# Performance work log

Hardware: AMD Instinct MI355X
Metric: run time of the kernel (lower is better)

Reference implementation:

```python
import jax, jax.numpy as jnp
import numpy as np

K = 3
TOPK = 10
HORIZON = 12


def gru_cell(x, h, w_ih, w_hh, b_ih, b_hh):
    # torch GRU gate order: r, z, n ; n = tanh(W_in x + b_in + r*(W_hn h + b_hn))
    gx = x @ w_ih.T + b_ih
    gh = h @ w_hh.T + b_hh
    H = h.shape[-1]
    r = jax.nn.sigmoid(gx[:, :H] + gh[:, :H])
    z = jax.nn.sigmoid(gx[:, H:2 * H] + gh[:, H:2 * H])
    n = jnp.tanh(gx[:, 2 * H:] + r * gh[:, 2 * H:])
    return (1.0 - z) * n + z * h


def setup_inputs() -> dict:
    key = jax.random.key(0)
    ks = jax.random.split(key, 16)
    B, T, N, F = 128, 12, 207, 14
    H = 128
    f = lambda i, shp, s=0.1: jax.random.normal(ks[i], shp, dtype=jnp.float32) * s
    return {
        'x': jax.random.normal(ks[0], (B, T, N, F), dtype=jnp.float32),
        'A_physical': jax.random.uniform(ks[1], (N, N), dtype=jnp.float32),
        'fc_start_w': f(2, (16, 1), 0.5),
        'fc_start_b': jnp.zeros((16,), jnp.float32),
        'alpha': jnp.float32(0.5),
        'context_w': f(3, (32, 13)),
        'context_b': jnp.zeros((32,), jnp.float32),
        'tcn_w': f(4, (64, 1, 1, 3), 0.3),
        'tcn_b': jnp.zeros((64,), jnp.float32),
        'theta': f(5, (K, 32, 32), 0.15),
        'attn_w': f(6, (1, 65)),
        'attn_b': jnp.zeros((1,), jnp.float32),
        'enc_w_ih': f(7, (3 * H, 65)),
        'enc_w_hh': f(8, (3 * H, H)),
        'enc_b_ih': jnp.zeros((3 * H,), jnp.float32),
        'enc_b_hh': jnp.zeros((3 * H,), jnp.float32),
        'dec_w_ih': f(9, (3 * H, 33)),
        'dec_w_hh': f(10, (3 * H, H)),
        'dec_b_ih': jnp.zeros((3 * H,), jnp.float32),
        'dec_b_hh': jnp.zeros((3 * H,), jnp.float32),
        'out_w': f(11, (1, H)),
        'out_b': jnp.zeros((1,), jnp.float32),
    }


def reference(x, A_physical, fc_start_w, fc_start_b, alpha, context_w, context_b,
              tcn_w, tcn_b, theta, attn_w, attn_b,
              enc_w_ih, enc_w_hh, enc_b_ih, enc_b_hh,
              dec_w_ih, dec_w_hh, dec_b_ih, dec_b_hh, out_w, out_b):
    B, T, N, _ = x.shape
    H = enc_w_hh.shape[1]
    traffic = x[..., 0:1]          # [B,T,N,1]
    context = x[..., 1:]           # [B,T,N,13]

    # ---- dynamic graph: topk + scatter + softmax, blended with physical ----
    state = traffic[:, -1]                                   # [B,N,1]
    emb = jnp.tanh(state @ fc_start_w.T + fc_start_b)        # [B,N,16]
    A_dyn = jax.nn.relu(jnp.einsum('bnd,bmd->bnm', emb, emb))
    vals, idx = jax.lax.top_k(A_dyn, TOPK)
    sparse = jnp.zeros_like(A_dyn).at[
        jnp.arange(B)[:, None, None], jnp.arange(N)[None, :, None], idx].set(vals)
    A_dyn = jax.nn.softmax(sparse, axis=2)
    a = jax.nn.sigmoid(alpha)
    A = a * A_physical[None] + (1.0 - a) * A_dyn             # [B,N,N]

    # ---- gated temporal conv (causal, GLU) ----
    xt = jnp.transpose(traffic, (0, 3, 2, 1))                # [B,1,N,T]
    conv = jax.lax.conv_general_dilated(
        xt, tcn_w, (1, 1), [(0, 0), (2, 0)],
        dimension_numbers=('NCHW', 'OIHW', 'NCHW')) + tcn_b[None, :, None, None]
    P, Q = jnp.split(conv, 2, axis=1)
    t_feat = jnp.transpose(P * jax.nn.sigmoid(Q), (0, 3, 2, 1))  # [B,T,N,32]

    # ---- Chebyshev K-hop graph conv ----
    I = jnp.eye(N, dtype=x.dtype)
    lam = jnp.clip(jnp.max(jnp.sum(A, -1), -1), 1.0)[:, None, None]
    L = 2.0 * A / lam - I[None]
    Tk = [jnp.broadcast_to(I[None], (B, N, N)), L]
    for k in range(2, K):
        Tk.append(2.0 * jnp.einsum('bnm,bmp->bnp', L, Tk[-1]) - Tk[-2])
    s = 0.0
    for k in range(K):
        rhs = jnp.einsum('btnf,fo->btno', t_feat, theta[k])
        s = s + jnp.einsum('bnm,btmo->btno', Tk[k], rhs)
    s_feat = jax.nn.relu(s)                                   # [B,T,N,32] (dropout off: eval)

    # ---- attention fusion ----
    c_emb = jax.nn.relu(context @ context_w.T + context_b)    # [B,T,N,32]
    fusion = jnp.concatenate([traffic, s_feat, c_emb], -1)    # [B,T,N,65]
    attn = jax.nn.sigmoid(fusion @ attn_w.T + attn_b)
    z = fusion * attn
    # NOTE: original torch code does z.view(B*N, T, -1) on a [B,T,N,65] contiguous
    # tensor (raw reshape, no permute) -- replicated faithfully.
    z_flat = z.reshape(B * N, T, -1)

    # ---- encoder GRU ----
    h = jnp.zeros((B * N, H), x.dtype)
    def enc_step(h, xt_):
        return gru_cell(xt_, h, enc_w_ih, enc_w_hh, enc_b_ih, enc_b_hh), None
    h, _ = jax.lax.scan(enc_step, h, jnp.transpose(z_flat, (1, 0, 2)))

    cur = traffic[:, -1, :, 0].reshape(B * N, 1)
    ctx = c_emb[:, -1].reshape(B * N, 32)
    def dec_step(carry, _):
        hh, cc = carry
        h2 = gru_cell(jnp.concatenate([cc, ctx], 1), hh,
                      dec_w_ih, dec_w_hh, dec_b_ih, dec_b_hh)
        pred = h2 @ out_w.T + out_b
        return (h2, pred), pred
    _, preds = jax.lax.scan(dec_step, (h, cur), None, length=HORIZON)  # [Hz,B*N,1]
    out = jnp.transpose(preds[..., 0], (1, 0)).reshape(B, N, HORIZON)
    return jnp.transpose(out, (0, 2, 1))                      # [B,horizon,N]
```

## Files before the change

### kernel.cpp

```cpp
#include <hip/hip_runtime.h>
#include <math.h>

#define NB 128
#define NT 12
#define NNODE 207
#define NF 14
#define NH 128
#define ROWS (NB*NNODE)
#define BTN (NB*NT*NNODE)
#define G3 (3*NH)
#define LSTR 208
#define RG (ROWS/16)

typedef __attribute__((ext_vector_type(8))) short short8;
typedef __attribute__((ext_vector_type(4))) float accf4;

#define MFMA16 __builtin_amdgcn_mfma_f32_16x16x32_bf16

__device__ __forceinline__ float sigf(float x){ return 1.0f/(1.0f+__expf(-x)); }
__device__ __forceinline__ unsigned short f2b(float f){
  unsigned int u = __float_as_uint(f);
  return (unsigned short)((u + 0x7FFFu + ((u>>16)&1u)) >> 16);
}
__device__ __forceinline__ float b2f(unsigned short h){
  return __uint_as_float(((unsigned int)h) << 16);
}
__device__ __forceinline__ void mm3(short8 ah, short8 al, short8 bh, short8 bl, accf4& acc){
  acc = MFMA16(ah, bh, acc, 0,0,0);
  acc = MFMA16(al, bh, acc, 0,0,0);
  acc = MFMA16(ah, bl, acc, 0,0,0);
}

__global__ __launch_bounds__(256) void k_sentinel(float* __restrict__ out, int n){
  int i = blockIdx.x*256 + threadIdx.x;
  if (i < n) out[i] = 12345.0f;
}

#define NW_ENC (7*24*64*8)
#define NW_DEC (4*24*64*8)
#define SH_TOTAL (2*NW_ENC + 2*NW_DEC)
#define FWT_TOTAL (32*384 + 384)
#define PREP_TOTAL (NW_ENC + NW_DEC + 32*384 + 384)
__global__ __launch_bounds__(256) void k_prep(const float* __restrict__ ewih,
    const float* __restrict__ ewhh, const float* __restrict__ dwih,
    const float* __restrict__ dwhh, short* __restrict__ ws, float* __restrict__ wf){
  int i = blockIdx.x*256 + threadIdx.x;
  if (i < NW_ENC){
    int e = i & 7, lane = (i>>3) & 63, ct = (i>>9) % 24, ks = i / 12288;
    int k = ks*32 + (lane>>4)*8 + e;
    int col = ct*16 + (lane&15);
    float wv = (k < 65) ? ewih[col*65 + k] : ((k < 96) ? 0.f : ewhh[col*128 + (k-96)]);
    unsigned short hi = f2b(wv);
    ws[i] = (short)hi;
    ws[NW_ENC + i] = (short)f2b(wv - b2f(hi));
  } else if (i < NW_ENC + NW_DEC){
    int j = i - NW_ENC;
    int e = j & 7, lane = (j>>3) & 63, ct = (j>>9) % 24, ks = j / 12288;
    int k = ks*32 + (lane>>4)*8 + e;
    int col = ct*16 + (lane&15);
    float wv = dwhh[col*128 + k];
    unsigned short hi = f2b(wv);
    ws[2*NW_ENC + j] = (short)hi;
    ws[2*NW_ENC + NW_DEC + j] = (short)f2b(wv - b2f(hi));
  } else if (i < NW_ENC + NW_DEC + 32*384){
    int j = i - (NW_ENC + NW_DEC); int k = j/384, n = j%384;
    wf[j] = dwih[n*33 + 1 + k];
  } else if (i < PREP_TOTAL){
    int n = i - (NW_ENC + NW_DEC + 32*384);
    wf[32*384 + n] = dwih[n*33];
  }
}

__global__ __launch_bounds__(256) void k_emb(const float* __restrict__ x,
    const float* __restrict__ w, const float* __restrict__ b, float* __restrict__ emb){
  int idx = blockIdx.x*256 + threadIdx.x;
  if (idx >= ROWS*16) return;
  int j = idx & 15, row = idx >> 4;
  int bb = row / NNODE, n = row % NNODE;
  float s = x[((bb*NT + (NT-1))*NNODE + n)*NF];
  emb[idx] = tanhf(s*w[j] + b[j]);
}

__global__ __launch_bounds__(256) void k_adj(const float* __restrict__ emb,
    const float* __restrict__ Aph, const float* __restrict__ alp,
    float* __restrict__ Abuf, float* __restrict__ rsum){
  int wid = threadIdx.x >> 6, lane = threadIdx.x & 63;
  int row = blockIdx.x*4 + wid;
  int bb = row / NNODE, n = row % NNODE;
  const float4* er = (const float4*)(emb + (size_t)row*16);
  float4 e0 = er[0], e1 = er[1], e2 = er[2], e3 = er[3];
  float d[4];
  #pragma unroll
  for (int q=0;q<4;++q){
    int m = lane + q*64;
    float dd = -1.f;
    if (m < NNODE){
      const float4* em = (const float4*)(emb + (size_t)(bb*NNODE+m)*16);
      float4 m0 = em[0], m1 = em[1], m2 = em[2], m3 = em[3];
      dd = e0.x*m0.x + e0.y*m0.y + e0.z*m0.z + e0.w*m0.w
         + e1.x*m1.x + e1.y*m1.y + e1.z*m1.z + e1.w*m1.w
         + e2.x*m2.x + e2.y*m2.y + e2.z*m2.z + e2.w*m2.w
         + e3.x*m3.x + e3.y*m3.y + e3.z*m3.z + e3.w*m3.w;
      dd = dd > 0.f ? dd : 0.f;
    }
    d[q] = dd;
  }
  int km = 0;
  float vmax = 0.f;
  for (int it=0; it<10; ++it){
    float v = -1.f; int mi = 1<<20;
    #pragma unroll
    for (int q=0;q<4;++q){
      if (d[q] >= 0.f && !((km>>q)&1) && d[q] > v){ v = d[q]; mi = lane + q*64; }
    }
    #pragma unroll
    for (int off=1; off<64; off<<=1){
      float v2 = __shfl_xor(v, off, 64);
      int  i2 = __shfl_xor(mi, off, 64);
      if (v2 > v || (v2 == v && i2 < mi)){ v = v2; mi = i2; }
    }
    if (it == 0) vmax = v;
    if ((mi & 63) == lane) km |= 1 << (mi >> 6);
  }
  float a = sigf(alp[0]);
  float eneg = __expf(-vmax);
  float p[4]; float ps = 0.f;
  #pragma unroll
  for (int q=0;q<4;++q){
    p[q] = 0.f;
    if (d[q] >= 0.f) p[q] = ((km>>q)&1) ? __expf(d[q]-vmax) : eneg;
    ps += p[q];
  }
  #pragma unroll
  for (int off=1; off<64; off<<=1) ps += __shfl_xor(ps, off, 64);
  float inv = (1.f - a)/ps;
  float rs = 0.f;
  #pragma unroll
  for (int q=0;q<4;++q){
    int m = lane + q*64;
    if (m < NNODE){
      float Av = a*Aph[n*NNODE + m] + p[q]*inv;
      Abuf[(size_t)row*LSTR + m] = Av;
      rs += Av;
    }
  }
  if (lane == 0) Abuf[(size_t)row*LSTR + 207] = 0.f;
  #pragma unroll
  for (int off=1; off<64; off<<=1) rs += __shfl_xor(rs, off, 64);
  if (lane == 0) rsum[row] = rs;
}

__global__ __launch_bounds__(256) void k_lam(const float* __restrict__ rsum, float* __restrict__ lam){
  __shared__ float rv[256];
  int b = blockIdx.x, tid = threadIdx.x;
  rv[tid] = (tid < NNODE) ? rsum[b*NNODE+tid] : -1e30f;
  __syncthreads();
  for (int s=128;s>0;s>>=1){ if (tid<s) rv[tid]=fmaxf(rv[tid],rv[tid+s]); __syncthreads(); }
  if (tid==0) lam[b] = fmaxf(rv[0], 1.0f);
}

__global__ __launch_bounds__(256) void k_lap(float* __restrict__ Abuf, const float* __restrict__ lam){
  int idx = blockIdx.x*256 + threadIdx.x;
  if (idx >= NB*NNODE*LSTR) return;
  int b = idx / (NNODE*LSTR);
  int rem = idx % (NNODE*LSTR);
  int n = rem / LSTR, m = rem % LSTR;
  Abuf[idx] = 2.f*Abuf[idx]/lam[b] - (n==m ? 1.f : 0.f);
}

__global__ __launch_bounds__(256) void k_tcn(const float* __restrict__ x,
    const float* __restrict__ w, const float* __restrict__ bcn, float* __restrict__ tfeat){
  int idx = blockIdx.x*256 + threadIdx.x;
  if (idx >= BTN*32) return;
  int o = idx & 31; int r = idx >> 5;
  int n = r % NNODE, bt = r / NNODE, t = bt % NT, b = bt / NT;
  float t0 = (t>=2)? x[((size_t)(b*NT+t-2)*NNODE+n)*NF] : 0.f;
  float t1 = (t>=1)? x[((size_t)(b*NT+t-1)*NNODE+n)*NF] : 0.f;
  float t2 = x[((size_t)(b*NT+t)*NNODE+n)*NF];
  float P = bcn[o]    + w[o*3]*t0       + w[o*3+1]*t1       + w[o*3+2]*t2;
  float Q = bcn[o+32] + w[(o+32)*3]*t0  + w[(o+32)*3+1]*t1  + w[(o+32)*3+2]*t2;
  tfeat[(size_t)r*32 + o] = P * sigf(Q);
}

__global__ __launch_bounds__(256) void k_thetaBC(const float* __restrict__ tfeat,
    const float* __restrict__ theta, float* __restrict__ P2, float* __restrict__ P1){
  __shared__ float thB[32][33], thC[32][33];
  __shared__ float tf[8][32];
  int tid = threadIdx.x;
  for (int i=tid; i<1024; i+=256){
    int f = i >> 5, o = i & 31;
    thB[o][f] = theta[1024+f*32+o]; thC[o][f] = theta[2048+f*32+o];
  }
  int rl = tid >> 5, o = tid & 31;
  int r = blockIdx.x*8 + rl;
  tf[rl][o] = tfeat[(size_t)r*32 + o];
  __syncthreads();
  float aB=0.f, aC=0.f;
  #pragma unroll
  for (int f=0; f<32; ++f){
    float t = tf[rl][f];
    aB += t*thB[o][f]; aC += t*thC[o][f];
  }
  int n = r % NNODE, bt = r / NNODE, t = bt % NT, b = bt / NT;
  size_t outi = (size_t)(b*NNODE+n)*G3 + t*32 + o;
  P2[outi]=aB; P1[outi]=aC;
}

__global__ __launch_bounds__(256) void k_thetaA(const float* __restrict__ tfeat,
    const float* __restrict__ theta, float* __restrict__ P1){
  __shared__ float thA[32][33];
  __shared__ float tf[8][32];
  int tid = threadIdx.x;
  for (int i=tid; i<1024; i+=256){
    int f = i >> 5, o = i & 31;
    thA[o][f] = theta[f*32+o] - theta[2048+f*32+o];
  }
  int rl = tid >> 5, o = tid & 31;
  int r = blockIdx.x*8 + rl;
  tf[rl][o] = tfeat[(size_t)r*32 + o];
  __syncthreads();
  float aA=0.f;
  #pragma unroll
  for (int f=0; f<32; ++f) aA += tf[rl][f]*thA[o][f];
  int n = r % NNODE, bt = r / NNODE, t = bt % NT, b = bt / NT;
  P1[(size_t)(b*NNODE+n)*G3 + t*32 + o] = aA;
}

__global__ __launch_bounds__(256) void gemm128(
    const float* __restrict__ Ab, int lda, long long sA,
    const float* __restrict__ Bb, long long sB,
    const float* __restrict__ bias,
    const float* __restrict__ Yb, long long sY, float alphaV, float betaV, int do_relu,
    float* __restrict__ Cb, long long sC, int M, int kchunks){
  __shared__ float As[16][132];
  __shared__ float Bs[16][132];
  int bz = blockIdx.z;
  const float* A = Ab + (size_t)bz*sA;
  const float* B = Bb + (size_t)bz*sB;
  float* C = Cb + (size_t)bz*sC;
  int n0 = blockIdx.x*128, m0 = blockIdx.y*128;
  int tid = threadIdx.x, tx = tid & 15, ty = tid >> 4;
  float acc[8][8] = {};
  int ar = tid & 127, ak = (tid >> 7)*8;
  int bk = tid >> 4, bn = (tid & 15)*8;
  for (int kc=0; kc<kchunks; ++kc){
    int k0 = kc*16;
    int m = m0 + ar;
    if (m < M){
      const float* ap = A + (size_t)m*lda + k0 + ak;
      float4 v0 = *(const float4*)ap, v1 = *(const float4*)(ap+4);
      As[ak+0][ar]=v0.x; As[ak+1][ar]=v0.y; As[ak+2][ar]=v0.z; As[ak+3][ar]=v0.w;
      As[ak+4][ar]=v1.x; As[ak+5][ar]=v1.y; As[ak+6][ar]=v1.z; As[ak+7][ar]=v1.w;
    } else {
      #pragma unroll
      for (int j=0;j<8;++j) As[ak+j][ar]=0.f;
    }
    const float* bp = B + (size_t)(k0+bk)*384 + n0 + bn;
    float4 w0_ = *(const float4*)bp, w1_ = *(const float4*)(bp+4);
    *(float4*)&Bs[bk][bn] = w0_; *(float4*)&Bs[bk][bn+4] = w1_;
    __syncthreads();
    #pragma unroll
    for (int kk=0;kk<16;++kk){
      float4 a0 = *(const float4*)&As[kk][ty*8];
      float4 a1 = *(const float4*)&As[kk][ty*8+4];
      float4 b0 = *(const float4*)&Bs[kk][tx*4];
      float4 b1 = *(const float4*)&Bs[kk][64+tx*4];
      float av[8] = {a0.x,a0.y,a0.z,a0.w,a1.x,a1.y,a1.z,a1.w};
      float bv[8] = {b0.x,b0.y,b0.z,b0.w,b1.x,b1.y,b1.z,b1.w};
      #pragma unroll
      for (int i=0;i<8;++i)
        #pragma unroll
        for (int j=0;j<8;++j) acc[i][j] += av[i]*bv[j];
    }
    __syncthreads();
  }
  if (bias){
    float bl[4], bh_[4];
    #pragma unroll
    for (int j=0;j<4;++j){ bl[j]=bias[n0+tx*4+j]; bh_[j]=bias[n0+64+tx*4+j]; }
    #pragma unroll
    for (int i=0;i<8;++i){
      int m2 = m0 + ty*8 + i; if (m2 >= M) continue;
      float4 s0, s1;
      s0.x=acc[i][0]+bl[0]; s0.y=acc[i][1]+bl[1]; s0.z=acc[i][2]+bl[2]; s0.w=acc[i][3]+bl[3];
      s1.x=acc[i][4]+bh_[0]; s1.y=acc[i][5]+bh_[1]; s1.z=acc[i][6]+bh_[2]; s1.w=acc[i][7]+bh_[3];
      *(float4*)&C[(size_t)m2*384 + n0 + tx*4] = s0;
      *(float4*)&C[(size_t)m2*384 + n0 + 64 + tx*4] = s1;
    }
  } else {
    const float* Y = Yb + (size_t)bz*sY;
    #pragma unroll
    for (int i=0;i<8;++i){
      int m2 = m0 + ty*8 + i; if (m2 >= M) continue;
      const float* yr = Y + (size_t)m2*384;
      float* cr = C + (size_t)m2*384;
      float4 y0 = *(const float4*)(yr + n0 + tx*4);
      float4 y1 = *(const float4*)(yr + n0 + 64 + tx*4);
      float4 s0, s1;
      s0.x = alphaV*acc[i][0] + betaV*y0.x; s0.y = alphaV*acc[i][1] + betaV*y0.y;
      s0.z = alphaV*acc[i][2] + betaV*y0.z; s0.w = alphaV*acc[i][3] + betaV*y0.w;
      s1.x = alphaV*acc[i][4] + betaV*y1.x; s1.y = alphaV*acc[i][5] + betaV*y1.y;
      s1.z = alphaV*acc[i][6] + betaV*y1.z; s1.w = alphaV*acc[i][7] + betaV*y1.w;
      if (do_relu){
        s0.x=fmaxf(s0.x,0.f); s0.y=fmaxf(s0.y,0.f); s0.z=fmaxf(s0.z,0.f); s0.w=fmaxf(s0.w,0.f);
        s1.x=fmaxf(s1.x,0.f); s1.y=fmaxf(s1.y,0.f); s1.z=fmaxf(s1.z,0.f); s1.w=fmaxf(s1.w,0.f);
      }
      *(float4*)(cr + n0 + tx*4) = s0;
      *(float4*)(cr + n0 + 64 + tx*4) = s1;
    }
  }
}

#define GATEB(WH, WL, KS) \
    const int ko = (KS)*24; \
    short8 bRh = *(const short8*)(WH + ((size_t)(ko + w)*64 + lane)*8); \
    short8 bZh = *(const short8*)(WH + ((size_t)(ko + 8 + w)*64 + lane)*8); \
    short8 bNh = *(const short8*)(WH + ((size_t)(ko + 16 + w)*64 + lane)*8); \
    short8 bRl = *(const short8*)(WL + ((size_t)(ko + w)*64 + lane)*8); \
    short8 bZl = *(const short8*)(WL + ((size_t)(ko + 8 + w)*64 + lane)*8); \
    short8 bNl = *(const short8*)(WL + ((size_t)(ko + 16 + w)*64 + lane)*8);

__global__ __launch_bounds__(512) void k_encdec(
    const short* __restrict__ zfH, const short* __restrict__ zfL,
    const short* __restrict__ WFH, const short* __restrict__ WFL,
    const float* __restrict__ bih, const float* __restrict__ bhh,
    const short* __restrict__ DFH, const short* __restrict__ DFL,
    const float* __restrict__ dbhh, const float* __restrict__ ctxGX,
    const float* __restrict__ w0, const float* __restrict__ ow,
    const float* __restrict__ ob, const float* __restrict__ pred0,
    float* __restrict__ preds_out){
  __shared__ __attribute__((aligned(16))) short hfH[4*512];
  __shared__ __attribute__((aligned(16))) short hfL[4*512];
  __shared__ float psl[8][16];
  __shared__ float predl[16];
  int R = blockIdx.x, m0 = R*16;
  int tid = threadIdx.x;
  int w = tid >> 6, lane = tid & 63;
  int g = lane >> 4, c = lane & 15;
  int j = (w<<4) + c;
  float hreg[4] = {};
  for (int i = tid; i < 2048; i += 512){ hfH[i] = 0; hfL[i] = 0; }
  if (tid < 16) predl[tid] = pred0[m0 + tid];
  int ksh = w >> 1, qh = 2*(w&1) + (c>>3), eh = c & 7;
  float birv = bih[j], bizv = bih[128+j], binv = bih[256+j];
  float bhrv = bhh[j], bhzv = bhh[128+j], bhnv = bhh[256+j];
  __syncthreads();

  for (int t = 0; t < NT; ++t){
    accf4 aR = {}, aZ = {}, aNZ = {}, aNH = {};
    #pragma unroll
    for (int ks=0; ks<3; ++ks){
      GATEB(WFH, WFL, ks);
      size_t zb = (((size_t)t*RG + R)*3 + ks)*512;
      short8 ah = *(const short8*)(zfH + zb + lane*8);
      short8 al = *(const short8*)(zfL + zb + lane*8);
      mm3(ah, al, bRh, bRl, aR);
      mm3(ah, al, bZh, bZl, aZ);
      mm3(ah, al, bNh, bNl, aNZ);
    }
    #pragma unroll
    for (int ks=3; ks<7; ++ks){
      GATEB(WFH, WFL, ks);
      short8 ah = *(const short8*)&hfH[(ks-3)*512 + lane*8];
      short8 al = *(const short8*)&hfL[(ks-3)*512 + lane*8];
      mm3(ah, al, bRh, bRl, aR);
      mm3(ah, al, bZh, bZl, aZ);
      mm3(ah, al, bNh, bNl, aNH);
    }
    __syncthreads();
    #pragma unroll
    for (int i=0;i<4;++i){
      float r_ = sigf(aR[i] + birv + bhrv);
      float z_ = sigf(aZ[i] + bizv + bhzv);
      float n_ = tanhf(aNZ[i] + binv + r_*(aNH[i] + bhnv));
      float hn = (1.f - z_)*n_ + z_*hreg[i];
      hreg[i] = hn;
      unsigned short hh = f2b(hn);
      int o = ksh*512 + ((g*4+i) + 16*qh)*8 + eh;
      hfH[o] = (short)hh;
      hfL[o] = (short)f2b(hn - b2f(hh));
    }
    __syncthreads();
  }

  float w0r = w0[j], w0z = w0[128+j], w0n = w0[256+j];
  float bhr = dbhh[j], bhz = dbhh[128+j], bhn = dbhh[256+j];
  float owj = ow[j];
  float obv = ob[0];
  for (int s = 0; s < NT; ++s){
    accf4 aR = {}, aZ = {}, aN = {};
    #pragma unroll
    for (int ks=0; ks<4; ++ks){
      GATEB(DFH, DFL, ks);
      short8 ah = *(const short8*)&hfH[ks*512 + lane*8];
      short8 al = *(const short8*)&hfL[ks*512 + lane*8];
      mm3(ah, al, bRh, bRl, aR);
      mm3(ah, al, bZh, bZl, aZ);
      mm3(ah, al, bNh, bNl, aN);
    }
    __syncthreads();
    #pragma unroll
    for (int i=0;i<4;++i){
      int row = g*4 + i;
      float p = predl[row];
      const float* gx = ctxGX + (size_t)(m0+row)*384;
      float r_ = sigf(gx[j]     + p*w0r + aR[i] + bhr);
      float z_ = sigf(gx[128+j] + p*w0z + aZ[i] + bhz);
      float n_ = tanhf(gx[256+j] + p*w0n + r_*(aN[i] + bhn));
      float hn = (1.f - z_)*n_ + z_*hreg[i];
      hreg[i] = hn;
      unsigned short hh = f2b(hn);
      int o = ksh*512 + (row + 16*qh)*8 + eh;
      hfH[o] = (short)hh;
      hfL[o] = (short)f2b(hn - b2f(hh));
      float psv = hn*owj;
      psv += __shfl_xor(psv, 1, 64);
      psv += __shfl_xor(psv, 2, 64);
      psv += __shfl_xor(psv, 4, 64);
      psv += __shfl_xor(psv, 8, 64);
      if (c == 0) psl[w][row] = psv;
    }
    __syncthreads();
    if (tid < 16){
      float sm = obv;
      #pragma unroll
      for (int w2=0; w2<8; ++w2) sm += psl[w2][tid];
      predl[tid] = sm;
      preds_out[(size_t)s*ROWS + m0 + tid] = sm;
    }
  }
}

__global__ __launch_bounds__(256) void k_zbuild(const float* __restrict__ x,
    const float* __restrict__ S, const float* __restrict__ cw, const float* __restrict__ cb,
    const float* __restrict__ aw, const float* __restrict__ ab,
    short* __restrict__ zfH, short* __restrict__ zfL,
    float* __restrict__ ctx, float* __restrict__ pred0){
  __shared__ float cwl[416];
  __shared__ float cbl[32];
  __shared__ float awl[65];
  int tid = threadIdx.x;
  for (int i=tid; i<416; i+=256) cwl[i] = cw[i];
  if (tid < 32) cbl[tid] = cb[tid];
  if (tid < 65) awl[tid] = aw[tid];
  __syncthreads();
  int wid = tid >> 6, sel = (tid >> 5) & 1, hl = tid & 31;
  int r = blockIdx.x*8 + wid*2 + sel;
  int n = r % NNODE, bt = r / NNODE, t = bt % NT, b = bt / NT;
  const float* xr = x + (size_t)r*NF;
  float x0 = xr[0];
  float s_ = cbl[hl];
  #pragma unroll
  for (int f=0; f<13; ++f) s_ += xr[1+f]*cwl[hl*13+f];
  float ce = s_ > 0.f ? s_ : 0.f;
  float sv = S[(size_t)(b*NNODE+n)*G3 + t*32 + hl];
  float part = sv*awl[1+hl] + ce*awl[33+hl] + (hl==0 ? x0*awl[0] : 0.f);
  part += __shfl_xor(part, 1, 64);
  part += __shfl_xor(part, 2, 64);
  part += __shfl_xor(part, 4, 64);
  part += __shfl_xor(part, 8, 64);
  part += __shfl_xor(part, 16, 64);
  float attn = sigf(part + ab[0]);
  int i_ = r / NT, tau = r % NT;
  int Rg = i_ >> 4, rowin = i_ & 15;
  size_t basez = (((size_t)tau*RG + Rg)*3)*512;
  #define ZPUT(L, V) do{ int l_=(L); int ks_=l_>>5, q_=(l_&31)>>3, e_=l_&7; \
      size_t o_ = basez + (size_t)ks_*512 + ((rowin + 16*q_)<<3) + e_; \
      float v_=(V); unsigned short hh_ = f2b(v_); \
      zfH[o_] = (short)hh_; zfL[o_] = (short)f2b(v_ - b2f(hh_)); }while(0)
  ZPUT(1+hl, sv*attn);
  ZPUT(33+hl, ce*attn);
  if (hl == 0) ZPUT(0, x0*attn);
  if (hl <= 30) ZPUT(65+hl, 0.f);
  #undef ZPUT
  if (t == NT-1){
    ctx[(size_t)(b*NNODE+n)*32 + hl] = ce;
    if (hl == 0) pred0[b*NNODE+n] = x0;
  }
}

__global__ __launch_bounds__(256) void k_out(const float* __restrict__ preds, float* __restrict__ out){
  int idx = blockIdx.x*256 + threadIdx.x;
  if (idx >= NT*ROWS) return;
  int n = idx % NNODE;
  int t2 = idx / NNODE;
  int hor = t2 % NT;
  int b = t2 / NT;
  out[idx] = preds[(size_t)hor*ROWS + b*NNODE + n];
}

extern "C" void kernel_launch(void* const* d_in, const int* in_sizes, int n_in,
                              void* d_out, int out_size, void* d_ws, size_t ws_size,
                              hipStream_t stream){
  const float* x     = (const float*)d_in[0];
  const float* Aph   = (const float*)d_in[1];
  const float* fcw   = (const float*)d_in[2];
  const float* fcb   = (const float*)d_in[3];
  const float* alp   = (const float*)d_in[4];
  const float* cw    = (const float*)d_in[5];
  const float* cb    = (const float*)d_in[6];
  const float* tw    = (const float*)d_in[7];
  const float* tb    = (const float*)d_in[8];
  const float* theta = (const float*)d_in[9];
  const float* aw    = (const float*)d_in[10];
  const float* ab    = (const float*)d_in[11];
  const float* ewih  = (const float*)d_in[12];
  const float* ewhh  = (const float*)d_in[13];
  const float* ebih  = (const float*)d_in[14];
  const float* ebhh  = (const float*)d_in[15];
  const float* dwih  = (const float*)d_in[16];
  const float* dwhh  = (const float*)d_in[17];
  const float* dbih  = (const float*)d_in[18];
  const float* dbhh  = (const float*)d_in[19];
  const float* ow    = (const float*)d_in[20];
  const float* ob    = (const float*)d_in[21];
  float* out = (float*)d_out;

  const size_t SZ_CTX  = (size_t)ROWS*32;
  const size_t SZ_PRED = (size_t)ROWS;
  const size_t SZ_PREDS= (size_t)NT*ROWS;
  const size_t SZ_G    = (size_t)ROWS*G3;
  const size_t SZ_ABUF = (size_t)NB*NNODE*LSTR;
  const size_t SZ_EMB  = (size_t)ROWS*16;
  const size_t SZ_ZF   = (size_t)NT*RG*3*512;
  const size_t SZ_UNION_FL = (2*SZ_ZF + 3) / 2;
  const size_t UNION_FL = (SZ_UNION_FL > 2*SZ_G) ? SZ_UNION_FL : 2*SZ_G;

  float* w = (float*)d_ws;
  size_t off = 0;
  auto alloc = [&](size_t nfl){ float* p = w + off; off += nfl; return p; };
  float* ctx   = alloc(SZ_CTX);
  float* pred  = alloc(SZ_PRED);
  float* preds = alloc(SZ_PREDS);
  float* Abuf  = alloc(SZ_ABUF);
  float* emb   = alloc(SZ_EMB);
  float* rsum  = alloc(SZ_PRED);
  float* lam   = alloc((size_t)NB);
  short* wS    = (short*)alloc(SH_TOTAL/2);
  float* wF    = alloc((size_t)FWT_TOTAL);
  float* Sslot = alloc(SZ_G);
  float* Uzone = alloc(UNION_FL);
  float* P1 = Uzone;
  float* P2 = Uzone + SZ_G;
  short* zfH = (short*)Uzone;
  short* zfL = zfH + SZ_ZF;
  (void)n_in; (void)in_sizes;

  if (ws_size < off*sizeof(float)){
    k_sentinel<<<(out_size+255)/256, 256, 0, stream>>>(out, out_size);
    return;
  }

  const short* WFH = wS;
  const short* WFL = wS + NW_ENC;
  const short* DFH = wS + 2*NW_ENC;
  const short* DFL = wS + 2*NW_ENC + NW_DEC;
  float* dwihT = wF;
  float* w0    = wF + 32*384;

  k_prep<<<(PREP_TOTAL+255)/256, 256, 0, stream>>>(ewih, ewhh, dwih, dwhh, wS, wF);
  float* tfeat = Sslot;
  k_emb<<<(ROWS*16)/256, 256, 0, stream>>>(x, fcw, fcb, emb);
  k_adj<<<ROWS/4, 256, 0, stream>>>(emb, Aph, alp, Abuf, rsum);
  k_lam<<<NB, 256, 0, stream>>>(rsum, lam);
  k_lap<<<(NB*NNODE*LSTR)/256, 256, 0, stream>>>(Abuf, lam);
  k_tcn<<<(BTN*32)/256, 256, 0, stream>>>(x, tw, tb, tfeat);
  k_thetaBC<<<BTN/8, 256, 0, stream>>>(tfeat, theta, P2, P1);
  gemm128<<<dim3(3, 2, NB), 256, 0, stream>>>(Abuf, LSTR, (long long)NNODE*LSTR,
      P1, (long long)NNODE*G3, nullptr,
      P2, (long long)NNODE*G3, 2.f, 1.f, 0,
      P2, (long long)NNODE*G3, NNODE, 13);
  k_thetaA<<<BTN/8, 256, 0, stream>>>(tfeat, theta, P1);
  gemm128<<<dim3(3, 2, NB), 256, 0, stream>>>(Abuf, LSTR, (long long)NNODE*LSTR,
      P2, (long long)NNODE*G3, nullptr,
      P1, (long long)NNODE*G3, 1.f, 1.f, 1,
      Sslot, (long long)NNODE*G3, NNODE, 13);
  k_zbuild<<<BTN/8, 256, 0, stream>>>(x, Sslot, cw, cb, aw, ab, zfH, zfL, ctx, pred);
  float* ctxGX = Sslot;
  gemm128<<<dim3(3, ROWS/128, 1), 256, 0, stream>>>(
      ctx, 32, 0, dwihT, 0, dbih,
      nullptr, 0, 1.f, 0.f, 0, ctxGX, 0, ROWS, 2);
  k_encdec<<<RG, 512, 0, stream>>>(zfH, zfL, WFH, WFL, ebih, ebhh,
      DFH, DFL, dbhh, ctxGX, w0, ow, ob, pred, preds);
  k_out<<<(NT*ROWS)/256, 256, 0, stream>>>(preds, out);
}
```

Measured before the change: 844.7 us.

## Stage z tiles in LDS for coalesced stores, hoist decoder gx loads, fast tanh

k_zbuild is remapped so each block builds one complete 16-row MFMA tile (one tau, one row group) in shared memory, then writes it out with coalesced 32-bit stores. This replaces the scattered per-element 16-bit global writes and the separate zero-padding writes. In the decoder, the per-row ctxGX gate inputs are loaded into registers once before the 12-step loop instead of being re-read every step. tanhf is replaced by an exp-based fast tanh in both GRU loops, which may lose a little accuracy and could overflow to inf for large inputs, though the formula still saturates correctly.

```diff
diff --git a/kernel.cpp b/kernel.cpp
--- a/kernel.cpp
+++ b/kernel.cpp
@@ -18,6 +18,10 @@
 #define MFMA16 __builtin_amdgcn_mfma_f32_16x16x32_bf16
 
 __device__ __forceinline__ float sigf(float x){ return 1.0f/(1.0f+__expf(-x)); }
+__device__ __forceinline__ float tanhfast(float x){
+  float e = __expf(2.f*x);
+  return 1.f - 2.f/(e + 1.f);
+}
 __device__ __forceinline__ unsigned short f2b(float f){
   unsigned int u = __float_as_uint(f);
   return (unsigned short)((u + 0x7FFFu + ((u>>16)&1u)) >> 16);
@@ -372,7 +376,7 @@
     for (int i=0;i<4;++i){
       float r_ = sigf(aR[i] + birv + bhrv);
       float z_ = sigf(aZ[i] + bizv + bhzv);
-      float n_ = tanhf(aNZ[i] + binv + r_*(aNH[i] + bhnv));
+      float n_ = tanhfast(aNZ[i] + binv + r_*(aNH[i] + bhnv));
       float hn = (1.f - z_)*n_ + z_*hreg[i];
       hreg[i] = hn;
       unsigned short hh = f2b(hn);
@@ -387,6 +391,13 @@
   float bhr = dbhh[j], bhz = dbhh[128+j], bhn = dbhh[256+j];
   float owj = ow[j];
   float obv = ob[0];
+  float gxr[4], gxz[4], gxn[4];
+  #pragma unroll
+  for (int i=0;i<4;++i){
+    int row = g*4 + i;
+    const float* gx = ctxGX + (size_t)(m0+row)*384;
+    gxr[i] = gx[j]; gxz[i] = gx[128+j]; gxn[i] = gx[256+j];
+  }
   for (int s = 0; s < NT; ++s){
     accf4 aR = {}, aZ = {}, aN = {};
     #pragma unroll
@@ -403,10 +414,9 @@
     for (int i=0;i<4;++i){
       int row = g*4 + i;
       float p = predl[row];
-      const float* gx = ctxGX + (size_t)(m0+row)*384;
-      float r_ = sigf(gx[j]     + p*w0r + aR[i] + bhr);
-      float z_ = sigf(gx[128+j] + p*w0z + aZ[i] + bhz);
-      float n_ = tanhf(gx[256+j] + p*w0n + r_*(aN[i] + bhn));
+      float r_ = sigf(gxr[i] + p*w0r + aR[i] + bhr);
+      float z_ = sigf(gxz[i] + p*w0z + aZ[i] + bhz);
+      float n_ = tanhfast(gxn[i] + p*w0n + r_*(aN[i] + bhn));
       float hn = (1.f - z_)*n_ + z_*hreg[i];
       hreg[i] = hn;
       unsigned short hh = f2b(hn);
@@ -439,44 +449,64 @@
   __shared__ float cwl[416];
   __shared__ float cbl[32];
   __shared__ float awl[65];
+  __shared__ short zH[1536];
+  __shared__ short zL[1536];
   int tid = threadIdx.x;
   for (int i=tid; i<416; i+=256) cwl[i] = cw[i];
   if (tid < 32) cbl[tid] = cb[tid];
   if (tid < 65) awl[tid] = aw[tid];
+  {
+    int* zHi = (int*)zH; int* zLi = (int*)zL;
+    for (int i=tid; i<768; i+=256){ zHi[i] = 0; zLi[i] = 0; }
+  }
   __syncthreads();
-  int wid = tid >> 6, sel = (tid >> 5) & 1, hl = tid & 31;
-  int r = blockIdx.x*8 + wid*2 + sel;
+  int bid = blockIdx.x;
+  int tau = bid / RG, Rg = bid % RG;
+  int trow = tid >> 4, tl = tid & 15;
+  int i_ = Rg*16 + trow;
+  int r = i_*NT + tau;
   int n = r % NNODE, bt = r / NNODE, t = bt % NT, b = bt / NT;
   const float* xr = x + (size_t)r*NF;
   float x0 = xr[0];
-  float s_ = cbl[hl];
-  #pragma unroll
-  for (int f=0; f<13; ++f) s_ += xr[1+f]*cwl[hl*13+f];
-  float ce = s_ > 0.f ? s_ : 0.f;
-  float sv = S[(size_t)(b*NNODE+n)*G3 + t*32 + hl];
-  float part = sv*awl[1+hl] + ce*awl[33+hl] + (hl==0 ? x0*awl[0] : 0.f);
+  float ce0 = cbl[tl], ce1 = cbl[tl+16];
+  #pragma unroll
+  for (int f=0; f<13; ++f){
+    float xv = xr[1+f];
+    ce0 += xv*cwl[tl*13+f];
+    ce1 += xv*cwl[(tl+16)*13+f];
+  }
+  ce0 = fmaxf(ce0, 0.f); ce1 = fmaxf(ce1, 0.f);
+  const float* sr = S + (size_t)(b*NNODE+n)*G3 + t*32;
+  float sv0 = sr[tl], sv1 = sr[tl+16];
+  float part = sv0*awl[1+tl] + ce0*awl[33+tl]
+             + sv1*awl[17+tl] + ce1*awl[49+tl]
+             + (tl==0 ? x0*awl[0] : 0.f);
   part += __shfl_xor(part, 1, 64);
   part += __shfl_xor(part, 2, 64);
   part += __shfl_xor(part, 4, 64);
   part += __shfl_xor(part, 8, 64);
-  part += __shfl_xor(part, 16, 64);
   float attn = sigf(part + ab[0]);
-  int i_ = r / NT, tau = r % NT;
-  int Rg = i_ >> 4, rowin = i_ & 15;
-  size_t basez = (((size_t)tau*RG + Rg)*3)*512;
   #define ZPUT(L, V) do{ int l_=(L); int ks_=l_>>5, q_=(l_&31)>>3, e_=l_&7; \
-      size_t o_ = basez + (size_t)ks_*512 + ((rowin + 16*q_)<<3) + e_; \
+      int o_ = ks_*512 + ((trow + 16*q_)<<3) + e_; \
       float v_=(V); unsigned short hh_ = f2b(v_); \
-      zfH[o_] = (short)hh_; zfL[o_] = (short)f2b(v_ - b2f(hh_)); }while(0)
-  ZPUT(1+hl, sv*attn);
-  ZPUT(33+hl, ce*attn);
-  if (hl == 0) ZPUT(0, x0*attn);
-  if (hl <= 30) ZPUT(65+hl, 0.f);
+      zH[o_] = (short)hh_; zL[o_] = (short)f2b(v_ - b2f(hh_)); }while(0)
+  ZPUT(1+tl, sv0*attn);
+  ZPUT(17+tl, sv1*attn);
+  ZPUT(33+tl, ce0*attn);
+  ZPUT(49+tl, ce1*attn);
+  if (tl == 0) ZPUT(0, x0*attn);
   #undef ZPUT
   if (t == NT-1){
-    ctx[(size_t)(b*NNODE+n)*32 + hl] = ce;
-    if (hl == 0) pred0[b*NNODE+n] = x0;
-  }
+    float* cr = ctx + (size_t)(b*NNODE+n)*32;
+    cr[tl] = ce0; cr[tl+16] = ce1;
+    if (tl == 0) pred0[b*NNODE+n] = x0;
+  }
+  __syncthreads();
+  size_t gb = (size_t)bid*1536;
+  const int* zHi = (const int*)zH; const int* zLi = (const int*)zL;
+  int* gH = (int*)(zfH + gb); int* gL = (int*)(zfL + gb);
+  #pragma unroll
+  for (int i=tid; i<768; i+=256){ gH[i] = zHi[i]; gL[i] = zLi[i]; }
 }
 
 __global__ __launch_bounds__(256) void k_out(const float* __restrict__ preds, float* __restrict__ out){
@@ -575,7 +605,7 @@
       P2, (long long)NNODE*G3, nullptr,
       P1, (long long)NNODE*G3, 1.f, 1.f, 1,
       Sslot, (long long)NNODE*G3, NNODE, 13);
-  k_zbuild<<<BTN/8, 256, 0, stream>>>(x, Sslot, cw, cb, aw, ab, zfH, zfL, ctx, pred);
+  k_zbuild<<<NT*RG, 256, 0, stream>>>(x, Sslot, cw, cb, aw, ab, zfH, zfL, ctx, pred);
   float* ctxGX = Sslot;
   gemm128<<<dim3(3, ROWS/128, 1), 256, 0, stream>>>(
       ctx, 32, 0, dwihT, 0, dbih,
```

Result: faster. 805.8 us (-4.6%).
